# Optimization experiments

Measured on AMD Instinct MI355X. Metric: run time of the kernel, lower is better.

## Reference

```python
import jax, jax.numpy as jnp
import numpy as np

N_NODES = 100000
N_EDGES = 1600000
IN_FEATS = 128
N_HIDDEN = 128
N_CLASSES = 64


def _degree_norms(src, dst, n_nodes):
    ones = jnp.ones(src.shape[0], dtype=jnp.float32)
    deg_out = jax.ops.segment_sum(ones, src, num_segments=n_nodes)  # out-degree of src nodes
    deg_in = jax.ops.segment_sum(ones, dst, num_segments=n_nodes)   # in-degree of dst nodes
    norm_src = jax.lax.rsqrt(jnp.clip(deg_out, 1.0))  # D_src^{-1/2}, clamp like DGL
    norm_dst = jax.lax.rsqrt(jnp.clip(deg_in, 1.0))   # D_dst^{-1/2}
    return norm_src, norm_dst


def _graph_conv(x, src, dst, norm_src, norm_dst, W, b, relu):
    # DGL GraphConv, norm='both': D_dst^{-1/2} A D_src^{-1/2} X W + b
    h = x * norm_src[:, None]
    agg = jax.ops.segment_sum(h[src], dst, num_segments=x.shape[0])  # [N, d]
    h = agg * norm_dst[:, None]
    h = h @ W + b
    return jax.nn.relu(h) if relu else h


def setup_inputs() -> dict:
    key = jax.random.key(0)
    ks = jax.random.split(key, 10)
    features = jax.random.normal(ks[0], (N_NODES, IN_FEATS), dtype=jnp.float32)
    src = jax.random.randint(ks[1], (N_EDGES,), 0, N_NODES, dtype=jnp.int64 if jax.config.read('jax_enable_x64') else jnp.int32)
    dst = jax.random.randint(ks[2], (N_EDGES,), 0, N_NODES, dtype=src.dtype)
    s = 1.0 / np.sqrt(IN_FEATS)
    W0 = jax.random.uniform(ks[3], (IN_FEATS, N_HIDDEN), jnp.float32, -s, s)
    b0 = jnp.zeros((N_HIDDEN,), jnp.float32)
    sh = 1.0 / np.sqrt(N_HIDDEN)
    W1 = jax.random.uniform(ks[4], (N_HIDDEN, N_HIDDEN), jnp.float32, -sh, sh)
    b1 = jnp.zeros((N_HIDDEN,), jnp.float32)
    W2 = jax.random.uniform(ks[5], (N_HIDDEN, N_CLASSES), jnp.float32, -sh, sh)
    b2 = jnp.zeros((N_CLASSES,), jnp.float32)
    return {"features": features, "src": src, "dst": dst,
            "W0": W0, "b0": b0, "W1": W1, "b1": b1, "W2": W2, "b2": b2}


def reference(features, src, dst, W0, b0, W1, b1, W2, b2):
    norm_src, norm_dst = _degree_norms(src, dst, features.shape[0])
    # dropout is identity in eval mode
    h = _graph_conv(features, src, dst, norm_src, norm_dst, W0, b0, relu=True)
    h = _graph_conv(h, src, dst, norm_src, norm_dst, W1, b1, relu=True)
    h = _graph_conv(h, src, dst, norm_src, norm_dst, W2, b2, relu=False)
    return h
```

## Files before the change

kernel.cpp:

```cpp
#include <hip/hip_runtime.h>
#include <hip/hip_fp16.h>

#define K_FEATS 128
#define RBSHIFT 9
#define RB 512

typedef short bf16x8 __attribute__((ext_vector_type(8)));
typedef float f32x4 __attribute__((ext_vector_type(4)));

__device__ __forceinline__ unsigned short bf16_rne(float x) {
    unsigned u = __float_as_uint(x);
    unsigned r = (u + 0x7FFFu + ((u >> 16) & 1u)) >> 16;
    return (unsigned short)r;
}
__device__ __forceinline__ float bf16_f(unsigned short h) {
    return __uint_as_float(((unsigned)h) << 16);
}

__global__ __launch_bounds__(256) void split_w3(
    const float* __restrict__ W0, const float* __restrict__ W1,
    const float* __restrict__ W2,
    unsigned short* __restrict__ W0th, unsigned short* __restrict__ W0tl,
    unsigned short* __restrict__ W1th, unsigned short* __restrict__ W1tl,
    unsigned short* __restrict__ W2th, unsigned short* __restrict__ W2tl)
{
    int e = blockIdx.x * 256 + threadIdx.x;
    const float* W;
    unsigned short *Wh, *Wl;
    int NC, idx;
    if (e < 16384)      { W = W0; Wh = W0th; Wl = W0tl; NC = 128; idx = e; }
    else if (e < 32768) { W = W1; Wh = W1th; Wl = W1tl; NC = 128; idx = e - 16384; }
    else if (e < 40960) { W = W2; Wh = W2th; Wl = W2tl; NC = 64;  idx = e - 32768; }
    else return;
    int c = idx >> 7, k = idx & 127;
    float w = W[k * NC + c];
    unsigned short h = bf16_rne(w);
    Wh[idx] = h;
    Wl[idx] = bf16_rne(w - bf16_f(h));
}

__global__ __launch_bounds__(256) void bucket_count(
    const int* __restrict__ src, const int* __restrict__ dst,
    int* __restrict__ partialS, int* __restrict__ partialD,
    int ne, int chunkA, int C, int NB)
{
    __shared__ int hS[256];
    __shared__ int hD[256];
    int c = blockIdx.x, t = threadIdx.x;
    if (t < NB) { hS[t] = 0; hD[t] = 0; }
    __syncthreads();
    int e0 = c * chunkA, e1 = min(ne, e0 + chunkA);
    for (int e = e0 + t; e < e1; e += 256) {
        atomicAdd(&hS[src[e] >> RBSHIFT], 1);
        atomicAdd(&hD[dst[e] >> RBSHIFT], 1);
    }
    __syncthreads();
    for (int i = t; i < NB; i += 256) {
        partialS[i * C + c] = hS[i];
        partialD[i * C + c] = hD[i];
    }
}

__global__ __launch_bounds__(256) void bucket_prefix(
    int* __restrict__ partialS, int* __restrict__ partialD,
    int* __restrict__ totS, int* __restrict__ totD, int C, int NB)
{
    __shared__ int sh[256];
    int b = blockIdx.x, t = threadIdx.x;
    int* part = blockIdx.y ? partialD : partialS;
    int* tot = blockIdx.y ? totD : totS;
    int v = (t < C) ? part[b * C + t] : 0;
    sh[t] = v;
    __syncthreads();
    for (int off = 1; off < 256; off <<= 1) {
        int x = (t >= off) ? sh[t - off] : 0;
        __syncthreads();
        sh[t] += x;
        __syncthreads();
    }
    if (t < C) part[b * C + t] = sh[t] - v;
    if (t == 255) tot[b] = sh[255];
}

__global__ __launch_bounds__(256) void bucket_off_kernel(
    const int* __restrict__ totS, const int* __restrict__ totD,
    int* __restrict__ offS, int* __restrict__ offD,
    int* __restrict__ row_off, int NB, int n, int ne)
{
    __shared__ int sh[256];
    int t = threadIdx.x;
    if (t == 0) row_off[n] = ne;
    for (int a = 0; a < 2; a++) {
        const int* tot = a ? totD : totS;
        int* boff = a ? offD : offS;
        int v = (t < NB) ? tot[t] : 0;
        sh[t] = v;
        __syncthreads();
        for (int off = 1; off < 256; off <<= 1) {
            int x = (t >= off) ? sh[t - off] : 0;
            __syncthreads();
            sh[t] += x;
            __syncthreads();
        }
        if (t < NB) boff[t] = sh[t] - v;
        if (t == NB - 1) boff[NB] = sh[t];
        __syncthreads();
    }
}

__global__ __launch_bounds__(256) void bucket_scatter(
    const int* __restrict__ src, const int* __restrict__ dst,
    const int* __restrict__ partialS, const int* __restrict__ partialD,
    const int* __restrict__ offS, const int* __restrict__ offD,
    unsigned short* __restrict__ src_bkt, int* __restrict__ edge_bkt,
    int ne, int chunkA, int C, int NB)
{
    __shared__ int curS[256];
    __shared__ int curD[256];
    int c = blockIdx.x, t = threadIdx.x;
    if (t < NB) {
        curS[t] = offS[t] + partialS[t * C + c];
        curD[t] = offD[t] + partialD[t * C + c];
    }
    __syncthreads();
    int e0 = c * chunkA, e1 = min(ne, e0 + chunkA);
    for (int e = e0 + t; e < e1; e += 256) {
        int s = src[e];
        int d = dst[e];
        int posD = atomicAdd(&curD[d >> RBSHIFT], 1);
        edge_bkt[posD] = ((d & (RB - 1)) << 17) | s;
        int posS = atomicAdd(&curS[s >> RBSHIFT], 1);
        src_bkt[posS] = (unsigned short)(s & (RB - 1));
    }
}

__global__ __launch_bounds__(256) void fine_all(
    const int* __restrict__ edge_bkt, const unsigned short* __restrict__ src_bkt,
    const int* __restrict__ offD, const int* __restrict__ offS,
    int* __restrict__ row_off, float* __restrict__ norm_dst,
    float* __restrict__ norm_src, int* __restrict__ csr, int n)
{
    __shared__ int h[RB];
    __shared__ int ps[256];
    int b = blockIdx.x, t = threadIdx.x;
    int lo = b << RBSHIFT;
    for (int i = t; i < RB; i += 256) h[i] = 0;
    __syncthreads();
    if (blockIdx.y == 1) {
        int e1 = offS[b + 1];
        for (int e = offS[b] + t; e < e1; e += 256)
            atomicAdd(&h[src_bkt[e]], 1);
        __syncthreads();
        for (int i = t; i < RB; i += 256) {
            int g = lo + i;
            if (g < n) norm_src[g] = rsqrtf((float)max(h[i], 1));
        }
        return;
    }
    int ebase = offD[b];
    int e1 = offD[b + 1];
    for (int e = ebase + t; e < e1; e += 256)
        atomicAdd(&h[(unsigned)edge_bkt[e] >> 17], 1);
    __syncthreads();
    int v0 = h[2 * t], v1 = h[2 * t + 1];
    ps[t] = v0 + v1;
    __syncthreads();
    for (int off = 1; off < 256; off <<= 1) {
        int x = (t >= off) ? ps[t - off] : 0;
        __syncthreads();
        ps[t] += x;
        __syncthreads();
    }
    int excl = ps[t] - (v0 + v1) + ebase;
    int g0 = lo + 2 * t, g1 = g0 + 1;
    if (g0 < n) { row_off[g0] = excl;      norm_dst[g0] = rsqrtf((float)max(v0, 1)); }
    if (g1 < n) { row_off[g1] = excl + v0; norm_dst[g1] = rsqrtf((float)max(v1, 1)); }
    h[2 * t] = excl;
    h[2 * t + 1] = excl + v0;
    __syncthreads();
    for (int e = ebase + t; e < e1; e += 256) {
        int p = edge_bkt[e];
        int pos = atomicAdd(&h[(unsigned)p >> 17], 1);
        csr[pos] = p & 0x1FFFF;
    }
}

template <int NCOL, bool HALF_OUT, int MODE>
__global__ __launch_bounds__(256) void gemm_mfma(
    const __half* __restrict__ X16, const float* __restrict__ Xf,
    const unsigned short* __restrict__ Wth, const unsigned short* __restrict__ Wtl,
    const float* __restrict__ scale, void* __restrict__ outv, int n)
{
    constexpr int CT = NCOL / 16;
    constexpr int CHUNKS = NCOL * 16;
    __shared__ unsigned short Ws[16 * NCOL * 8];

    int t = threadIdx.x;
    int w = t >> 6, lane = t & 63, m = lane & 15, q = lane >> 4;
    int r0 = blockIdx.x * 128 + w * 32;

    f32x4 acc[2][CT];
#pragma unroll
    for (int i = 0; i < 2; i++)
#pragma unroll
        for (int j = 0; j < CT; j++) acc[i][j] = (f32x4){0.f, 0.f, 0.f, 0.f};

    bf16x8 ah[2][4], al[2][4];
#pragma unroll
    for (int rt = 0; rt < 2; rt++) {
        int row = r0 + rt * 16 + m;
        size_t base = (size_t)row * K_FEATS + q * 8;
#pragma unroll
        for (int k = 0; k < 4; k++) {
            float f[8];
            if (MODE == 0) {
                if (row < n) {
                    *(float4*)&f[0] = *(const float4*)(Xf + base + k * 32);
                    *(float4*)&f[4] = *(const float4*)(Xf + base + k * 32 + 4);
                } else {
#pragma unroll
                    for (int j = 0; j < 8; j++) f[j] = 0.f;
                }
            } else {
                union { uint4 q4; __half h[8]; } U;
                U.q4 = *(const uint4*)(X16 + base + k * 32);
#pragma unroll
                for (int j = 0; j < 8; j++) f[j] = __half2float(U.h[j]);
            }
            union { bf16x8 v; unsigned short u[8]; } H, L;
#pragma unroll
            for (int j = 0; j < 8; j++) {
                H.u[j] = bf16_rne(f[j]);
                L.u[j] = bf16_rne(f[j] - bf16_f(H.u[j]));
            }
            ah[rt][k] = H.v;
            al[rt][k] = L.v;
        }
    }

#pragma unroll
    for (int i = 0; i < CHUNKS / 256; i++) {
        int g = t + i * 256;
        int col = g >> 4, sec = g & 15;
        *(bf16x8*)(Ws + sec * NCOL * 8 + ((col ^ (sec & 7)) * 8)) =
            *(const bf16x8*)(Wth + g * 8);
    }
    __syncthreads();
#pragma unroll
    for (int k = 0; k < 4; k++) {
        int sec = k * 4 + q;
#pragma unroll
        for (int ct = 0; ct < CT; ct++) {
            bf16x8 bh = *(const bf16x8*)(Ws + sec * NCOL * 8 +
                                         (((ct * 16 + m) ^ (sec & 7)) * 8));
            acc[0][ct] = __builtin_amdgcn_mfma_f32_16x16x32_bf16(ah[0][k], bh, acc[0][ct], 0, 0, 0);
            acc[0][ct] = __builtin_amdgcn_mfma_f32_16x16x32_bf16(al[0][k], bh, acc[0][ct], 0, 0, 0);
            acc[1][ct] = __builtin_amdgcn_mfma_f32_16x16x32_bf16(ah[1][k], bh, acc[1][ct], 0, 0, 0);
            acc[1][ct] = __builtin_amdgcn_mfma_f32_16x16x32_bf16(al[1][k], bh, acc[1][ct], 0, 0, 0);
        }
    }
    __syncthreads();
#pragma unroll
    for (int i = 0; i < CHUNKS / 256; i++) {
        int g = t + i * 256;
        int col = g >> 4, sec = g & 15;
        *(bf16x8*)(Ws + sec * NCOL * 8 + ((col ^ (sec & 7)) * 8)) =
            *(const bf16x8*)(Wtl + g * 8);
    }
    __syncthreads();
#pragma unroll
    for (int k = 0; k < 4; k++) {
        int sec = k * 4 + q;
#pragma unroll
        for (int ct = 0; ct < CT; ct++) {
            bf16x8 bl = *(const bf16x8*)(Ws + sec * NCOL * 8 +
                                         (((ct * 16 + m) ^ (sec & 7)) * 8));
            acc[0][ct] = __builtin_amdgcn_mfma_f32_16x16x32_bf16(ah[0][k], bl, acc[0][ct], 0, 0, 0);
            acc[1][ct] = __builtin_amdgcn_mfma_f32_16x16x32_bf16(ah[1][k], bl, acc[1][ct], 0, 0, 0);
        }
    }

#pragma unroll
    for (int rt = 0; rt < 2; rt++) {
        int rb = r0 + rt * 16 + q * 4;
#pragma unroll
        for (int reg = 0; reg < 4; reg++) {
            int row = rb + reg;
            if (row < n) {
                float s = scale[row];
#pragma unroll
                for (int ct = 0; ct < CT; ct++) {
                    float v = acc[rt][ct][reg] * s;
                    size_t o = (size_t)row * NCOL + ct * 16 + m;
                    if (HALF_OUT) ((__half*)outv)[o] = __float2half(v);
                    else ((float*)outv)[o] = v;
                }
            }
        }
    }
}

template <bool RELU>
__global__ __launch_bounds__(256) void aggregate4h(
    const __half* __restrict__ Tm, const int* __restrict__ row_off,
    const int* __restrict__ csr, const float* __restrict__ ndst,
    const float* __restrict__ bias, __half* __restrict__ Oh, int n)
{
    int lane = threadIdx.x & 15;
    int team = threadIdx.x >> 4;
    int fb = lane * 8;
    float b[8];
    *(float4*)&b[0] = *(const float4*)(bias + fb);
    *(float4*)&b[4] = *(const float4*)(bias + fb + 4);
    int stride = gridDim.x * 16;
    for (int v = blockIdx.x * 16 + team; v < n; v += stride) {
        int s = row_off[v], e = row_off[v + 1];
        float nd = ndst[v];
        float a[8] = {};
        int i = s;
        for (; i + 4 <= e; i += 4) {
            int u0 = csr[i], u1 = csr[i + 1], u2 = csr[i + 2], u3 = csr[i + 3];
            union { uint4 q; __half h[8]; } U0, U1, U2, U3;
            U0.q = *(const uint4*)(Tm + (size_t)u0 * 128 + fb);
            U1.q = *(const uint4*)(Tm + (size_t)u1 * 128 + fb);
            U2.q = *(const uint4*)(Tm + (size_t)u2 * 128 + fb);
            U3.q = *(const uint4*)(Tm + (size_t)u3 * 128 + fb);
#pragma unroll
            for (int j = 0; j < 8; j++)
                a[j] += (__half2float(U0.h[j]) + __half2float(U1.h[j])) +
                        (__half2float(U2.h[j]) + __half2float(U3.h[j]));
        }
        for (; i < e; i++) {
            int u = csr[i];
            union { uint4 q; __half h[8]; } U;
            U.q = *(const uint4*)(Tm + (size_t)u * 128 + fb);
#pragma unroll
            for (int j = 0; j < 8; j++) a[j] += __half2float(U.h[j]);
        }
        union { uint4 q; __half h[8]; } O;
#pragma unroll
        for (int j = 0; j < 8; j++) {
            float o = nd * a[j] + b[j];
            if (RELU) o = fmaxf(o, 0.f);
            O.h[j] = __float2half(o);
        }
        *(uint4*)(Oh + (size_t)v * 128 + fb) = O.q;
    }
}

__global__ __launch_bounds__(256) void aggregate2h(
    const __half* __restrict__ Tm, const int* __restrict__ row_off,
    const int* __restrict__ csr, const float* __restrict__ ndst,
    const float* __restrict__ bias, float* __restrict__ out, int n)
{
    int lane = threadIdx.x & 7;
    int team = threadIdx.x >> 3;
    int fb = lane * 8;
    float b[8];
    *(float4*)&b[0] = *(const float4*)(bias + fb);
    *(float4*)&b[4] = *(const float4*)(bias + fb + 4);
    int stride = gridDim.x * 32;
    for (int v = blockIdx.x * 32 + team; v < n; v += stride) {
        int s = row_off[v], e = row_off[v + 1];
        float nd = ndst[v];
        float a[8] = {};
        int i = s;
        for (; i + 4 <= e; i += 4) {
            int u0 = csr[i], u1 = csr[i + 1], u2 = csr[i + 2], u3 = csr[i + 3];
            union { uint4 q; __half h[8]; } U0, U1, U2, U3;
            U0.q = *(const uint4*)(Tm + (size_t)u0 * 64 + fb);
            U1.q = *(const uint4*)(Tm + (size_t)u1 * 64 + fb);
            U2.q = *(const uint4*)(Tm + (size_t)u2 * 64 + fb);
            U3.q = *(const uint4*)(Tm + (size_t)u3 * 64 + fb);
#pragma unroll
            for (int j = 0; j < 8; j++)
                a[j] += (__half2float(U0.h[j]) + __half2float(U1.h[j])) +
                        (__half2float(U2.h[j]) + __half2float(U3.h[j]));
        }
        for (; i < e; i++) {
            int u = csr[i];
            union { uint4 q; __half h[8]; } U;
            U.q = *(const uint4*)(Tm + (size_t)u * 64 + fb);
#pragma unroll
            for (int j = 0; j < 8; j++) a[j] += __half2float(U.h[j]);
        }
        float o[8];
#pragma unroll
        for (int j = 0; j < 8; j++) o[j] = nd * a[j] + b[j];
        *(float4*)(out + (size_t)v * 64 + fb) = *(float4*)&o[0];
        *(float4*)(out + (size_t)v * 64 + fb + 4) = *(float4*)&o[4];
    }
}

extern "C" void kernel_launch(void* const* d_in, const int* in_sizes, int n_in,
                              void* d_out, int out_size, void* d_ws, size_t ws_size,
                              hipStream_t stream)
{
    const float* features = (const float*)d_in[0];
    const int* src = (const int*)d_in[1];
    const int* dst = (const int*)d_in[2];
    const float* W0 = (const float*)d_in[3];
    const float* b0 = (const float*)d_in[4];
    const float* W1 = (const float*)d_in[5];
    const float* b1 = (const float*)d_in[6];
    const float* W2 = (const float*)d_in[7];
    const float* b2 = (const float*)d_in[8];

    int n = in_sizes[0] / K_FEATS;
    int ne = in_sizes[1];
    int n_pad = (n + 127) & ~127;

    char* ws = (char*)d_ws;
    size_t off = 0;
    auto take = [&](size_t bytes) -> char* {
        char* p = ws + off;
        off = (off + bytes + 255) & ~(size_t)255;
        return p;
    };
    __half* Xbuf = (__half*)take((size_t)n_pad * 128 * 2);
    __half* Th = (__half*)take((size_t)n_pad * 128 * 2);
    int* csr = (int*)take((size_t)ne * 4);
    int* edge_bkt = (int*)take((size_t)ne * 4);
    unsigned short* src_bkt = (unsigned short*)take((size_t)ne * 2);
    int* row_off = (int*)take((size_t)(n + 1) * 4);
    float* norm_src = (float*)take((size_t)n * 4);
    float* norm_dst = (float*)take((size_t)n * 4);
    unsigned short* W0th = (unsigned short*)take(128 * 128 * 2);
    unsigned short* W0tl = (unsigned short*)take(128 * 128 * 2);
    unsigned short* W1th = (unsigned short*)take(128 * 128 * 2);
    unsigned short* W1tl = (unsigned short*)take(128 * 128 * 2);
    unsigned short* W2th = (unsigned short*)take(64 * 128 * 2);
    unsigned short* W2tl = (unsigned short*)take(64 * 128 * 2);

    int NB = (n + RB - 1) >> RBSHIFT;
    int chunkA = 8192;
    int C = (ne + chunkA - 1) / chunkA;
    if (C > 256) { chunkA = (ne + 255) / 256; C = (ne + chunkA - 1) / chunkA; }

    int* partialS = (int*)take((size_t)NB * C * 4);
    int* partialD = (int*)take((size_t)NB * C * 4);
    int* totS = (int*)take((size_t)NB * 4);
    int* totD = (int*)take((size_t)NB * 4);
    int* offS = (int*)take((size_t)(NB + 1) * 4);
    int* offD = (int*)take((size_t)(NB + 1) * 4);

    split_w3<<<160, 256, 0, stream>>>(W0, W1, W2, W0th, W0tl, W1th, W1tl, W2th, W2tl);

    bucket_count<<<C, 256, 0, stream>>>(src, dst, partialS, partialD,
                                        ne, chunkA, C, NB);
    bucket_prefix<<<dim3(NB, 2), 256, 0, stream>>>(partialS, partialD, totS, totD, C, NB);
    bucket_off_kernel<<<1, 256, 0, stream>>>(totS, totD, offS, offD, row_off, NB, n, ne);
    bucket_scatter<<<C, 256, 0, stream>>>(src, dst, partialS, partialD,
                                          offS, offD, src_bkt, edge_bkt,
                                          ne, chunkA, C, NB);
    fine_all<<<dim3(NB, 2), 256, 0, stream>>>(edge_bkt, src_bkt, offD, offS,
                                              row_off, norm_dst, norm_src, csr, n);

    int gblocks = n_pad / 128;
    int ablocks4 = (n + 15) / 16;
    int ablocks2 = (n + 31) / 32;

    gemm_mfma<128, true, 0><<<gblocks, 256, 0, stream>>>(
        nullptr, features, W0th, W0tl, norm_src, Th, n);
    aggregate4h<true><<<ablocks4, 256, 0, stream>>>(Th, row_off, csr, norm_dst, b0,
                                                    Xbuf, n);
    gemm_mfma<128, true, 1><<<gblocks, 256, 0, stream>>>(
        Xbuf, nullptr, W1th, W1tl, norm_src, Th, n);
    aggregate4h<true><<<ablocks4, 256, 0, stream>>>(Th, row_off, csr, norm_dst, b1,
                                                    Xbuf, n);
    gemm_mfma<64, true, 1><<<gblocks, 256, 0, stream>>>(
        Xbuf, nullptr, W2th, W2tl, norm_src, Th, n);
    aggregate2h<<<ablocks2, 256, 0, stream>>>(Th, row_off, csr, norm_dst, b2,
                                              (float*)d_out, n);
}
```

Measured before the change: 374.9 us.

## Fuse CSR build preprocessing kernels into one persistent kernel with grid barriers

Merges the weight split, bucket count, prefix, offset, scatter and fine-CSR kernels into one persistent 512-block kernel. The phases are separated by software grid barriers built on atomics and spin-waiting, and each block recomputes the bucket offset scans redundantly in shared memory. The aim is to remove several kernel launch gaps and tiny single-block kernels. The risks are spin-barrier overhead, a possible deadlock if all 512 blocks are not co-resident, and reduced parallelism in phases that used more blocks.

```diff
diff --git a/kernel.cpp b/kernel.cpp
--- a/kernel.cpp
+++ b/kernel.cpp
@@ -4,6 +4,7 @@
 #define K_FEATS 128
 #define RBSHIFT 9
 #define RB 512
+#define GRID_PERS 512
 
 typedef short bf16x8 __attribute__((ext_vector_type(8)));
 typedef float f32x4 __attribute__((ext_vector_type(4)));
@@ -17,171 +18,180 @@
     return __uint_as_float(((unsigned)h) << 16);
 }
 
-__global__ __launch_bounds__(256) void split_w3(
+__device__ __forceinline__ void gbar(unsigned* bar, unsigned k) {
+    __syncthreads();
+    if (threadIdx.x == 0) {
+        __threadfence();
+        if (atomicAdd(&bar[k], 1u) == GRID_PERS - 1u) {
+            __threadfence();
+            atomicAdd(&bar[0], 1u);
+        } else {
+            while (atomicAdd(&bar[0], 0u) < k) __builtin_amdgcn_s_sleep(2);
+        }
+        __threadfence();
+    }
+    __syncthreads();
+}
+
+__global__ __launch_bounds__(256) void csr_build_all(
     const float* __restrict__ W0, const float* __restrict__ W1,
     const float* __restrict__ W2,
     unsigned short* __restrict__ W0th, unsigned short* __restrict__ W0tl,
     unsigned short* __restrict__ W1th, unsigned short* __restrict__ W1tl,
-    unsigned short* __restrict__ W2th, unsigned short* __restrict__ W2tl)
-{
-    int e = blockIdx.x * 256 + threadIdx.x;
-    const float* W;
-    unsigned short *Wh, *Wl;
-    int NC, idx;
-    if (e < 16384)      { W = W0; Wh = W0th; Wl = W0tl; NC = 128; idx = e; }
-    else if (e < 32768) { W = W1; Wh = W1th; Wl = W1tl; NC = 128; idx = e - 16384; }
-    else if (e < 40960) { W = W2; Wh = W2th; Wl = W2tl; NC = 64;  idx = e - 32768; }
-    else return;
-    int c = idx >> 7, k = idx & 127;
-    float w = W[k * NC + c];
-    unsigned short h = bf16_rne(w);
-    Wh[idx] = h;
-    Wl[idx] = bf16_rne(w - bf16_f(h));
-}
-
-__global__ __launch_bounds__(256) void bucket_count(
+    unsigned short* __restrict__ W2th, unsigned short* __restrict__ W2tl,
     const int* __restrict__ src, const int* __restrict__ dst,
     int* __restrict__ partialS, int* __restrict__ partialD,
-    int ne, int chunkA, int C, int NB)
+    int* __restrict__ totS, int* __restrict__ totD,
+    unsigned short* __restrict__ src_bkt, int* __restrict__ edge_bkt,
+    int* __restrict__ row_off, float* __restrict__ norm_dst,
+    float* __restrict__ norm_src, int* __restrict__ csr,
+    unsigned* __restrict__ bar,
+    int n, int ne, int chunkA, int C, int NB)
 {
-    __shared__ int hS[256];
-    __shared__ int hD[256];
-    int c = blockIdx.x, t = threadIdx.x;
-    if (t < NB) { hS[t] = 0; hD[t] = 0; }
-    __syncthreads();
-    int e0 = c * chunkA, e1 = min(ne, e0 + chunkA);
-    for (int e = e0 + t; e < e1; e += 256) {
-        atomicAdd(&hS[src[e] >> RBSHIFT], 1);
-        atomicAdd(&hD[dst[e] >> RBSHIFT], 1);
-    }
-    __syncthreads();
-    for (int i = t; i < NB; i += 256) {
-        partialS[i * C + c] = hS[i];
-        partialD[i * C + c] = hD[i];
-    }
-}
-
-__global__ __launch_bounds__(256) void bucket_prefix(
-    int* __restrict__ partialS, int* __restrict__ partialD,
-    int* __restrict__ totS, int* __restrict__ totD, int C, int NB)
-{
-    __shared__ int sh[256];
-    int b = blockIdx.x, t = threadIdx.x;
-    int* part = blockIdx.y ? partialD : partialS;
-    int* tot = blockIdx.y ? totD : totS;
-    int v = (t < C) ? part[b * C + t] : 0;
-    sh[t] = v;
-    __syncthreads();
-    for (int off = 1; off < 256; off <<= 1) {
-        int x = (t >= off) ? sh[t - off] : 0;
-        __syncthreads();
-        sh[t] += x;
-        __syncthreads();
-    }
-    if (t < C) part[b * C + t] = sh[t] - v;
-    if (t == 255) tot[b] = sh[255];
-}
-
-__global__ __launch_bounds__(256) void bucket_off_kernel(
-    const int* __restrict__ totS, const int* __restrict__ totD,
-    int* __restrict__ offS, int* __restrict__ offD,
-    int* __restrict__ row_off, int NB, int n, int ne)
-{
-    __shared__ int sh[256];
-    int t = threadIdx.x;
-    if (t == 0) row_off[n] = ne;
-    for (int a = 0; a < 2; a++) {
-        const int* tot = a ? totD : totS;
-        int* boff = a ? offD : offS;
-        int v = (t < NB) ? tot[t] : 0;
-        sh[t] = v;
-        __syncthreads();
-        for (int off = 1; off < 256; off <<= 1) {
-            int x = (t >= off) ? sh[t - off] : 0;
-            __syncthreads();
-            sh[t] += x;
-            __syncthreads();
-        }
-        if (t < NB) boff[t] = sh[t] - v;
-        if (t == NB - 1) boff[NB] = sh[t];
-        __syncthreads();
-    }
-}
-
-__global__ __launch_bounds__(256) void bucket_scatter(
-    const int* __restrict__ src, const int* __restrict__ dst,
-    const int* __restrict__ partialS, const int* __restrict__ partialD,
-    const int* __restrict__ offS, const int* __restrict__ offD,
-    unsigned short* __restrict__ src_bkt, int* __restrict__ edge_bkt,
-    int ne, int chunkA, int C, int NB)
-{
+    __shared__ int shA[RB];
+    __shared__ int shB[256];
     __shared__ int curS[256];
     __shared__ int curD[256];
-    int c = blockIdx.x, t = threadIdx.x;
-    if (t < NB) {
-        curS[t] = offS[t] + partialS[t * C + c];
-        curD[t] = offD[t] + partialD[t * C + c];
-    }
-    __syncthreads();
-    int e0 = c * chunkA, e1 = min(ne, e0 + chunkA);
-    for (int e = e0 + t; e < e1; e += 256) {
-        int s = src[e];
-        int d = dst[e];
-        int posD = atomicAdd(&curD[d >> RBSHIFT], 1);
-        edge_bkt[posD] = ((d & (RB - 1)) << 17) | s;
-        int posS = atomicAdd(&curS[s >> RBSHIFT], 1);
-        src_bkt[posS] = (unsigned short)(s & (RB - 1));
-    }
-}
-
-__global__ __launch_bounds__(256) void fine_all(
-    const int* __restrict__ edge_bkt, const unsigned short* __restrict__ src_bkt,
-    const int* __restrict__ offD, const int* __restrict__ offS,
-    int* __restrict__ row_off, float* __restrict__ norm_dst,
-    float* __restrict__ norm_src, int* __restrict__ csr, int n)
-{
-    __shared__ int h[RB];
-    __shared__ int ps[256];
-    int b = blockIdx.x, t = threadIdx.x;
-    int lo = b << RBSHIFT;
-    for (int i = t; i < RB; i += 256) h[i] = 0;
-    __syncthreads();
-    if (blockIdx.y == 1) {
-        int e1 = offS[b + 1];
-        for (int e = offS[b] + t; e < e1; e += 256)
-            atomicAdd(&h[src_bkt[e]], 1);
-        __syncthreads();
-        for (int i = t; i < RB; i += 256) {
-            int g = lo + i;
-            if (g < n) norm_src[g] = rsqrtf((float)max(h[i], 1));
-        }
-        return;
-    }
-    int ebase = offD[b];
-    int e1 = offD[b + 1];
-    for (int e = ebase + t; e < e1; e += 256)
-        atomicAdd(&h[(unsigned)edge_bkt[e] >> 17], 1);
-    __syncthreads();
-    int v0 = h[2 * t], v1 = h[2 * t + 1];
-    ps[t] = v0 + v1;
-    __syncthreads();
-    for (int off = 1; off < 256; off <<= 1) {
-        int x = (t >= off) ? ps[t - off] : 0;
-        __syncthreads();
-        ps[t] += x;
-        __syncthreads();
-    }
-    int excl = ps[t] - (v0 + v1) + ebase;
-    int g0 = lo + 2 * t, g1 = g0 + 1;
-    if (g0 < n) { row_off[g0] = excl;      norm_dst[g0] = rsqrtf((float)max(v0, 1)); }
-    if (g1 < n) { row_off[g1] = excl + v0; norm_dst[g1] = rsqrtf((float)max(v1, 1)); }
-    h[2 * t] = excl;
-    h[2 * t + 1] = excl + v0;
-    __syncthreads();
-    for (int e = ebase + t; e < e1; e += 256) {
-        int p = edge_bkt[e];
-        int pos = atomicAdd(&h[(unsigned)p >> 17], 1);
-        csr[pos] = p & 0x1FFFF;
+    int bid = blockIdx.x, t = threadIdx.x;
+
+    if (bid < C) {
+        if (t < NB) { shA[t] = 0; shB[t] = 0; }
+        __syncthreads();
+        int e0 = bid * chunkA, e1 = min(ne, e0 + chunkA);
+        for (int e = e0 + t; e < e1; e += 256) {
+            atomicAdd(&shA[src[e] >> RBSHIFT], 1);
+            atomicAdd(&shB[dst[e] >> RBSHIFT], 1);
+        }
+        __syncthreads();
+        for (int i = t; i < NB; i += 256) {
+            partialS[i * C + bid] = shA[i];
+            partialD[i * C + bid] = shB[i];
+        }
+    } else if (bid < C + 160) {
+        int e = (bid - C) * 256 + t;
+        const float* W; unsigned short *Wh, *Wl; int NC, idx;
+        bool ok = true;
+        if (e < 16384)      { W = W0; Wh = W0th; Wl = W0tl; NC = 128; idx = e; }
+        else if (e < 32768) { W = W1; Wh = W1th; Wl = W1tl; NC = 128; idx = e - 16384; }
+        else if (e < 40960) { W = W2; Wh = W2th; Wl = W2tl; NC = 64;  idx = e - 32768; }
+        else ok = false;
+        if (ok) {
+            int c = idx >> 7, kk = idx & 127;
+            float w = W[kk * NC + c];
+            unsigned short h = bf16_rne(w);
+            Wh[idx] = h;
+            Wl[idx] = bf16_rne(w - bf16_f(h));
+        }
+    }
+    gbar(bar, 1);
+
+    if (bid < 2 * NB) {
+        int b = bid >> 1;
+        int* part = (bid & 1) ? partialS : partialD;
+        int* tot  = (bid & 1) ? totS : totD;
+        int v = (t < C) ? part[b * C + t] : 0;
+        shB[t] = v;
+        __syncthreads();
+        for (int off = 1; off < 256; off <<= 1) {
+            int x = (t >= off) ? shB[t - off] : 0;
+            __syncthreads();
+            shB[t] += x;
+            __syncthreads();
+        }
+        if (t < C) part[b * C + t] = shB[t] - v;
+        if (t == 255) tot[b] = shB[255];
+    }
+    gbar(bar, 2);
+
+    if (bid < C) {
+        int vS = (t < NB) ? totS[t] : 0;
+        shB[t] = vS;
+        __syncthreads();
+        for (int off = 1; off < 256; off <<= 1) {
+            int x = (t >= off) ? shB[t - off] : 0;
+            __syncthreads();
+            shB[t] += x;
+            __syncthreads();
+        }
+        if (t < NB) curS[t] = (shB[t] - vS) + partialS[t * C + bid];
+        __syncthreads();
+        int vD = (t < NB) ? totD[t] : 0;
+        shB[t] = vD;
+        __syncthreads();
+        for (int off = 1; off < 256; off <<= 1) {
+            int x = (t >= off) ? shB[t - off] : 0;
+            __syncthreads();
+            shB[t] += x;
+            __syncthreads();
+        }
+        if (t < NB) curD[t] = (shB[t] - vD) + partialD[t * C + bid];
+        __syncthreads();
+        int e0 = bid * chunkA, e1 = min(ne, e0 + chunkA);
+        for (int e = e0 + t; e < e1; e += 256) {
+            int s = src[e];
+            int d = dst[e];
+            int posD = atomicAdd(&curD[d >> RBSHIFT], 1);
+            edge_bkt[posD] = ((d & (RB - 1)) << 17) | s;
+            int posS = atomicAdd(&curS[s >> RBSHIFT], 1);
+            src_bkt[posS] = (unsigned short)(s & (RB - 1));
+        }
+    }
+    gbar(bar, 3);
+
+    if (bid >= 2 * NB) return;
+    {
+        int y = bid & 1, b = bid >> 1;
+        const int* tot = y ? totS : totD;
+        int v = (t < NB) ? tot[t] : 0;
+        shB[t] = v;
+        __syncthreads();
+        for (int off = 1; off < 256; off <<= 1) {
+            int x = (t >= off) ? shB[t - off] : 0;
+            __syncthreads();
+            shB[t] += x;
+            __syncthreads();
+        }
+        int e1 = shB[b];
+        int ebase = e1 - tot[b];
+        __syncthreads();
+        int lo = b << RBSHIFT;
+        for (int i = t; i < RB; i += 256) shA[i] = 0;
+        __syncthreads();
+        if (y == 1) {
+            for (int e = ebase + t; e < e1; e += 256)
+                atomicAdd(&shA[src_bkt[e]], 1);
+            __syncthreads();
+            for (int i = t; i < RB; i += 256) {
+                int g = lo + i;
+                if (g < n) norm_src[g] = rsqrtf((float)max(shA[i], 1));
+            }
+            return;
+        }
+        if (bid == 0 && t == 0) row_off[n] = ne;
+        for (int e = ebase + t; e < e1; e += 256)
+            atomicAdd(&shA[(unsigned)edge_bkt[e] >> 17], 1);
+        __syncthreads();
+        int v0 = shA[2 * t], v1 = shA[2 * t + 1];
+        shB[t] = v0 + v1;
+        __syncthreads();
+        for (int off = 1; off < 256; off <<= 1) {
+            int x = (t >= off) ? shB[t - off] : 0;
+            __syncthreads();
+            shB[t] += x;
+            __syncthreads();
+        }
+        int excl = shB[t] - (v0 + v1) + ebase;
+        int g0 = lo + 2 * t, g1 = g0 + 1;
+        if (g0 < n) { row_off[g0] = excl;      norm_dst[g0] = rsqrtf((float)max(v0, 1)); }
+        if (g1 < n) { row_off[g1] = excl + v0; norm_dst[g1] = rsqrtf((float)max(v1, 1)); }
+        shA[2 * t] = excl;
+        shA[2 * t + 1] = excl + v0;
+        __syncthreads();
+        for (int e = ebase + t; e < e1; e += 256) {
+            int p = edge_bkt[e];
+            int pos = atomicAdd(&shA[(unsigned)p >> 17], 1);
+            csr[pos] = p & 0x1FFFF;
+        }
     }
 }
 
@@ -417,6 +427,7 @@
         off = (off + bytes + 255) & ~(size_t)255;
         return p;
     };
+    unsigned* bar = (unsigned*)take(256);
     __half* Xbuf = (__half*)take((size_t)n_pad * 128 * 2);
     __half* Th = (__half*)take((size_t)n_pad * 128 * 2);
     int* csr = (int*)take((size_t)ne * 4);
@@ -441,20 +452,13 @@
     int* partialD = (int*)take((size_t)NB * C * 4);
     int* totS = (int*)take((size_t)NB * 4);
     int* totD = (int*)take((size_t)NB * 4);
-    int* offS = (int*)take((size_t)(NB + 1) * 4);
-    int* offD = (int*)take((size_t)(NB + 1) * 4);
-
-    split_w3<<<160, 256, 0, stream>>>(W0, W1, W2, W0th, W0tl, W1th, W1tl, W2th, W2tl);
-
-    bucket_count<<<C, 256, 0, stream>>>(src, dst, partialS, partialD,
-                                        ne, chunkA, C, NB);
-    bucket_prefix<<<dim3(NB, 2), 256, 0, stream>>>(partialS, partialD, totS, totD, C, NB);
-    bucket_off_kernel<<<1, 256, 0, stream>>>(totS, totD, offS, offD, row_off, NB, n, ne);
-    bucket_scatter<<<C, 256, 0, stream>>>(src, dst, partialS, partialD,
-                                          offS, offD, src_bkt, edge_bkt,
-                                          ne, chunkA, C, NB);
-    fine_all<<<dim3(NB, 2), 256, 0, stream>>>(edge_bkt, src_bkt, offD, offS,
-                                              row_off, norm_dst, norm_src, csr, n);
+
+    hipMemsetAsync(bar, 0, 256, stream);
+    csr_build_all<<<GRID_PERS, 256, 0, stream>>>(
+        W0, W1, W2, W0th, W0tl, W1th, W1tl, W2th, W2tl,
+        src, dst, partialS, partialD, totS, totD,
+        src_bkt, edge_bkt, row_off, norm_dst, norm_src, csr, bar,
+        n, ne, chunkA, C, NB);
 
     int gblocks = n_pad / 128;
     int ablocks4 = (n + 15) / 16;
```

New measurement: 502.2 us. 33.9% more time.
